# Performance work log

Hardware: AMD Instinct MI355X
Metric: run time of the kernel (lower is better)

Reference implementation:

```python
import jax, jax.numpy as jnp
import numpy as np


def setup_inputs() -> dict:
    key = jax.random.key(0)
    k1, k2 = jax.random.split(key)
    B, T, D = 32, 8192, 256
    enc_hid_states = jax.random.normal(k1, (B, T, D), dtype=jnp.float32)
    dec_hid = jax.random.normal(k2, (B, D), dtype=jnp.float32)
    return {"enc_hid_states": enc_hid_states, "dec_hid": dec_hid}


def reference(enc_hid_states, dec_hid):
    # scores[b, t] = dec_hid[b] . enc_hid_states[b, t]
    scores = jnp.einsum("btd,bd->bt", enc_hid_states, dec_hid)
    align = jax.nn.softmax(scores, axis=1)            # [B, T]
    c_t = jnp.einsum("bt,btd->bd", align, enc_hid_states)  # [B, D]
    return c_t
```

## Files before the change

kernel.cpp:

```cpp
#include <hip/hip_runtime.h>
#include <math.h>


#define WAVES_PER_BLOCK 4
#define BLOCK 256
#define D 256

__global__ __launch_bounds__(BLOCK) void attn_partial(
    const float* __restrict__ enc,
    const float* __restrict__ dec,
    float* __restrict__ ws,
    int T, int P, int nblk_total)
{
    const int blk   = blockIdx.x;
    const int b     = blk / P;
    const int chunk = blk % P;
    const int tid   = threadIdx.x;
    const int wave  = tid >> 6;
    const int lane  = tid & 63;

    const int rows_per_block = T / P;
    const int rows_per_wave  = rows_per_block / WAVES_PER_BLOCK;
    const int t0 = chunk * rows_per_block + wave * rows_per_wave;

    const float* __restrict__ encb = enc + (size_t)b * T * D;

    const float4 dq = *reinterpret_cast<const float4*>(dec + b * D + lane * 4);

    float  m = -INFINITY;
    float  l = 0.0f;
    float4 acc = {0.0f, 0.0f, 0.0f, 0.0f};

    for (int r = 0; r < rows_per_wave; ++r) {
        const int t = t0 + r;
        const float4 x = *reinterpret_cast<const float4*>(encb + (size_t)t * D + lane * 4);
        float p = dq.x * x.x + dq.y * x.y + dq.z * x.z + dq.w * x.w;
        #pragma unroll
        for (int off = 32; off >= 1; off >>= 1)
            p += __shfl_xor(p, off, 64);
        const float mn    = fmaxf(m, p);
        const float scale = __expf(m - mn);
        const float w     = __expf(p - mn);
        acc.x = acc.x * scale + w * x.x;
        acc.y = acc.y * scale + w * x.y;
        acc.z = acc.z * scale + w * x.z;
        acc.w = acc.w * scale + w * x.w;
        l = l * scale + w;
        m = mn;
    }

    __shared__ float s_acc[WAVES_PER_BLOCK][D];
    __shared__ float s_m[WAVES_PER_BLOCK];
    __shared__ float s_l[WAVES_PER_BLOCK];

    *reinterpret_cast<float4*>(&s_acc[wave][lane * 4]) = acc;
    if (lane == 0) { s_m[wave] = m; s_l[wave] = l; }
    __syncthreads();

    if (wave == 0) {
        const float M = fmaxf(fmaxf(s_m[0], s_m[1]), fmaxf(s_m[2], s_m[3]));
        float4 a = {0.0f, 0.0f, 0.0f, 0.0f};
        float  L = 0.0f;
        #pragma unroll
        for (int wv = 0; wv < WAVES_PER_BLOCK; ++wv) {
            const float e = __expf(s_m[wv] - M);
            const float4 aw = *reinterpret_cast<const float4*>(&s_acc[wv][lane * 4]);
            a.x += e * aw.x; a.y += e * aw.y; a.z += e * aw.z; a.w += e * aw.w;
            L += e * s_l[wv];
        }
        float* pacc = ws + (size_t)blk * D;
        *reinterpret_cast<float4*>(pacc + lane * 4) = a;
        if (lane == 0) {
            float* ml = ws + (size_t)nblk_total * D;
            ml[blk * 2 + 0] = M;
            ml[blk * 2 + 1] = L;
        }
    }
}

__global__ __launch_bounds__(BLOCK) void attn_combine(
    const float* __restrict__ ws,
    float* __restrict__ out,
    int P, int nblk_total)
{
    const int b = blockIdx.x;
    const int d = threadIdx.x;
    const float* __restrict__ ml = ws + (size_t)nblk_total * D;

    float M = -INFINITY;
    for (int i = 0; i < P; ++i)
        M = fmaxf(M, ml[(b * P + i) * 2 + 0]);

    float a = 0.0f, L = 0.0f;
    for (int i = 0; i < P; ++i) {
        const int blk = b * P + i;
        const float e = __expf(ml[blk * 2 + 0] - M);
        a += e * ws[(size_t)blk * D + d];
        L += e * ml[blk * 2 + 1];
    }
    out[b * D + d] = a / L;
}

extern "C" void kernel_launch(void* const* d_in, const int* in_sizes, int n_in,
                              void* d_out, int out_size, void* d_ws, size_t ws_size,
                              hipStream_t stream) {
    const float* enc = (const float*)d_in[0];
    const float* dec = (const float*)d_in[1];
    float* out = (float*)d_out;
    float* ws  = (float*)d_ws;

    const int B = in_sizes[1] / D;
    const int T = in_sizes[0] / in_sizes[1];

    int P = 64;
    while (P > 1 && ((size_t)B * P * (D + 2) * sizeof(float)) > ws_size) P >>= 1;
    while (P > 1 && (T % (P * WAVES_PER_BLOCK) != 0)) P >>= 1;

    const int nblk = B * P;
    attn_partial<<<nblk, BLOCK, 0, stream>>>(enc, dec, ws, T, P, nblk);
    attn_combine<<<B, BLOCK, 0, stream>>>(ws, out, P, nblk);
}
```

Measured before the change: 68.42 us.

## Process four rows per wave with 16-lane groups and per-wave partials

Each wave is split into four 16-lane groups that each handle one row per iteration, so a wave loads four rows at once. The 64-lane dot-product shuffle chain shrinks to four shuffles. Rows are interleaved across waves, and each wave writes its own partial after a cross-group shuffle merge, which removes the shared-memory block reduction and the __syncthreads. The combine kernel now splits columns across four blocks per batch and slices the partials across waves. In exchange the partial kernel uses more registers (launch bounds 8), and the combine stage has four times as many partials to read.

Result: slower. 84.75 us (+23.9%).

```diff
diff --git a/kernel.cpp b/kernel.cpp
--- a/kernel.cpp
+++ b/kernel.cpp
@@ -2,15 +2,16 @@
 #include <math.h>
 
 
-#define WAVES_PER_BLOCK 4
 #define BLOCK 256
 #define D 256
+#define WPB 4
+#define ROWS_PER_ITER 16
 
-__global__ __launch_bounds__(BLOCK) void attn_partial(
+__global__ __launch_bounds__(BLOCK, 8) void attn_partial(
     const float* __restrict__ enc,
     const float* __restrict__ dec,
     float* __restrict__ ws,
-    int T, int P, int nblk_total)
+    int T, int P, int nw_total)
 {
     const int blk   = blockIdx.x;
     const int b     = blk / P;
@@ -18,87 +19,132 @@
     const int tid   = threadIdx.x;
     const int wave  = tid >> 6;
     const int lane  = tid & 63;
+    const int g     = lane >> 4;
+    const int k     = lane & 15;
 
     const int rows_per_block = T / P;
-    const int rows_per_wave  = rows_per_block / WAVES_PER_BLOCK;
-    const int t0 = chunk * rows_per_block + wave * rows_per_wave;
+    const int iters = rows_per_block / ROWS_PER_ITER;
+    const int base = chunk * rows_per_block + wave * 4 + g;
 
     const float* __restrict__ encb = enc + (size_t)b * T * D;
+    const float* __restrict__ decb = dec + (size_t)b * D;
 
-    const float4 dq = *reinterpret_cast<const float4*>(dec + b * D + lane * 4);
+    const float4 dq0 = *reinterpret_cast<const float4*>(decb + 0 * 64 + k * 4);
+    const float4 dq1 = *reinterpret_cast<const float4*>(decb + 1 * 64 + k * 4);
+    const float4 dq2 = *reinterpret_cast<const float4*>(decb + 2 * 64 + k * 4);
+    const float4 dq3 = *reinterpret_cast<const float4*>(decb + 3 * 64 + k * 4);
 
     float  m = -INFINITY;
     float  l = 0.0f;
-    float4 acc = {0.0f, 0.0f, 0.0f, 0.0f};
+    float4 a0 = {0,0,0,0}, a1 = {0,0,0,0}, a2 = {0,0,0,0}, a3 = {0,0,0,0};
 
-    for (int r = 0; r < rows_per_wave; ++r) {
-        const int t = t0 + r;
-        const float4 x = *reinterpret_cast<const float4*>(encb + (size_t)t * D + lane * 4);
-        float p = dq.x * x.x + dq.y * x.y + dq.z * x.z + dq.w * x.w;
-        #pragma unroll
-        for (int off = 32; off >= 1; off >>= 1)
-            p += __shfl_xor(p, off, 64);
+    const float* rowp = encb + (size_t)base * D + k * 4;
+
+    for (int i = 0; i < iters; ++i) {
+        const float* rp = rowp + (size_t)i * ROWS_PER_ITER * D;
+        const float4 x0 = *reinterpret_cast<const float4*>(rp + 0 * 64);
+        const float4 x1 = *reinterpret_cast<const float4*>(rp + 1 * 64);
+        const float4 x2 = *reinterpret_cast<const float4*>(rp + 2 * 64);
+        const float4 x3 = *reinterpret_cast<const float4*>(rp + 3 * 64);
+
+        float p = x0.x*dq0.x + x0.y*dq0.y + x0.z*dq0.z + x0.w*dq0.w;
+        p = fmaf(x1.x, dq1.x, fmaf(x1.y, dq1.y, fmaf(x1.z, dq1.z, fmaf(x1.w, dq1.w, p))));
+        p = fmaf(x2.x, dq2.x, fmaf(x2.y, dq2.y, fmaf(x2.z, dq2.z, fmaf(x2.w, dq2.w, p))));
+        p = fmaf(x3.x, dq3.x, fmaf(x3.y, dq3.y, fmaf(x3.z, dq3.z, fmaf(x3.w, dq3.w, p))));
+
+        p += __shfl_xor(p, 1, 64);
+        p += __shfl_xor(p, 2, 64);
+        p += __shfl_xor(p, 4, 64);
+        p += __shfl_xor(p, 8, 64);
+
         const float mn    = fmaxf(m, p);
         const float scale = __expf(m - mn);
         const float w     = __expf(p - mn);
-        acc.x = acc.x * scale + w * x.x;
-        acc.y = acc.y * scale + w * x.y;
-        acc.z = acc.z * scale + w * x.z;
-        acc.w = acc.w * scale + w * x.w;
-        l = l * scale + w;
+
+        a0.x = fmaf(w, x0.x, a0.x * scale); a0.y = fmaf(w, x0.y, a0.y * scale);
+        a0.z = fmaf(w, x0.z, a0.z * scale); a0.w = fmaf(w, x0.w, a0.w * scale);
+        a1.x = fmaf(w, x1.x, a1.x * scale); a1.y = fmaf(w, x1.y, a1.y * scale);
+        a1.z = fmaf(w, x1.z, a1.z * scale); a1.w = fmaf(w, x1.w, a1.w * scale);
+        a2.x = fmaf(w, x2.x, a2.x * scale); a2.y = fmaf(w, x2.y, a2.y * scale);
+        a2.z = fmaf(w, x2.z, a2.z * scale); a2.w = fmaf(w, x2.w, a2.w * scale);
+        a3.x = fmaf(w, x3.x, a3.x * scale); a3.y = fmaf(w, x3.y, a3.y * scale);
+        a3.z = fmaf(w, x3.z, a3.z * scale); a3.w = fmaf(w, x3.w, a3.w * scale);
+        l = fmaf(l, scale, w);
         m = mn;
     }
 
-    __shared__ float s_acc[WAVES_PER_BLOCK][D];
-    __shared__ float s_m[WAVES_PER_BLOCK];
-    __shared__ float s_l[WAVES_PER_BLOCK];
+    float M = fmaxf(m, __shfl_xor(m, 16, 64));
+    M = fmaxf(M, __shfl_xor(M, 32, 64));
+    const float e = __expf(m - M);
+    l *= e;
+    a0.x *= e; a0.y *= e; a0.z *= e; a0.w *= e;
+    a1.x *= e; a1.y *= e; a1.z *= e; a1.w *= e;
+    a2.x *= e; a2.y *= e; a2.z *= e; a2.w *= e;
+    a3.x *= e; a3.y *= e; a3.z *= e; a3.w *= e;
 
-    *reinterpret_cast<float4*>(&s_acc[wave][lane * 4]) = acc;
-    if (lane == 0) { s_m[wave] = m; s_l[wave] = l; }
-    __syncthreads();
+    l += __shfl_xor(l, 16, 64); l += __shfl_xor(l, 32, 64);
+#define RED2(c) c += __shfl_xor(c, 16, 64); c += __shfl_xor(c, 32, 64)
+    RED2(a0.x); RED2(a0.y); RED2(a0.z); RED2(a0.w);
+    RED2(a1.x); RED2(a1.y); RED2(a1.z); RED2(a1.w);
+    RED2(a2.x); RED2(a2.y); RED2(a2.z); RED2(a2.w);
+    RED2(a3.x); RED2(a3.y); RED2(a3.z); RED2(a3.w);
+#undef RED2
 
-    if (wave == 0) {
-        const float M = fmaxf(fmaxf(s_m[0], s_m[1]), fmaxf(s_m[2], s_m[3]));
-        float4 a = {0.0f, 0.0f, 0.0f, 0.0f};
-        float  L = 0.0f;
-        #pragma unroll
-        for (int wv = 0; wv < WAVES_PER_BLOCK; ++wv) {
-            const float e = __expf(s_m[wv] - M);
-            const float4 aw = *reinterpret_cast<const float4*>(&s_acc[wv][lane * 4]);
-            a.x += e * aw.x; a.y += e * aw.y; a.z += e * aw.z; a.w += e * aw.w;
-            L += e * s_l[wv];
-        }
-        float* pacc = ws + (size_t)blk * D;
-        *reinterpret_cast<float4*>(pacc + lane * 4) = a;
-        if (lane == 0) {
-            float* ml = ws + (size_t)nblk_total * D;
-            ml[blk * 2 + 0] = M;
-            ml[blk * 2 + 1] = L;
-        }
+    const float4 lo = (g & 1) ? a1 : a0;
+    const float4 hi = (g & 1) ? a3 : a2;
+    const float4 v  = (g & 2) ? hi : lo;
+
+    const int wid = blk * WPB + wave;
+    *reinterpret_cast<float4*>(ws + (size_t)wid * D + lane * 4) = v;
+    if (lane == 0) {
+        float* ml = ws + (size_t)nw_total * D;
+        ml[wid * 2 + 0] = M;
+        ml[wid * 2 + 1] = l;
     }
 }
 
 __global__ __launch_bounds__(BLOCK) void attn_combine(
     const float* __restrict__ ws,
     float* __restrict__ out,
-    int P, int nblk_total)
+    int nw, int nw_total)
 {
-    const int b = blockIdx.x;
-    const int d = threadIdx.x;
-    const float* __restrict__ ml = ws + (size_t)nblk_total * D;
+    const int b     = blockIdx.x >> 2;
+    const int cq    = blockIdx.x & 3;
+    const int tid   = threadIdx.x;
+    const int lane  = tid & 63;
+    const int slice = tid >> 6;
+    const int col   = cq * 64 + lane;
+    const int i0    = b * nw;
 
-    float M = -INFINITY;
-    for (int i = 0; i < P; ++i)
-        M = fmaxf(M, ml[(b * P + i) * 2 + 0]);
+    const float* __restrict__ ml = ws + (size_t)nw_total * D;
+
+    __shared__ float sM[4];
+    __shared__ float sL[4];
+    __shared__ float sA[4][64];
+
+    float Mw = -INFINITY;
+    for (int i = slice; i < nw; i += 4)
+        Mw = fmaxf(Mw, ml[(i0 + i) * 2 + 0]);
+    if (lane == 0) sM[slice] = Mw;
+    __syncthreads();
+    const float M = fmaxf(fmaxf(sM[0], sM[1]), fmaxf(sM[2], sM[3]));
 
     float a = 0.0f, L = 0.0f;
-    for (int i = 0; i < P; ++i) {
-        const int blk = b * P + i;
-        const float e = __expf(ml[blk * 2 + 0] - M);
-        a += e * ws[(size_t)blk * D + d];
-        L += e * ml[blk * 2 + 1];
+    for (int i = slice; i < nw; i += 4) {
+        const int pid = i0 + i;
+        const float e = __expf(ml[pid * 2 + 0] - M);
+        a = fmaf(e, ws[(size_t)pid * D + col], a);
+        L = fmaf(e, ml[pid * 2 + 1], L);
     }
-    out[b * D + d] = a / L;
+    sA[slice][lane] = a;
+    if (lane == 0) sL[slice] = L;
+    __syncthreads();
+
+    if (slice == 0) {
+        const float at = sA[0][lane] + sA[1][lane] + sA[2][lane] + sA[3][lane];
+        const float Lt = sL[0] + sL[1] + sL[2] + sL[3];
+        out[b * D + col] = at / Lt;
+    }
 }
 
 extern "C" void kernel_launch(void* const* d_in, const int* in_sizes, int n_in,
@@ -113,10 +159,11 @@
     const int T = in_sizes[0] / in_sizes[1];
 
     int P = 64;
-    while (P > 1 && ((size_t)B * P * (D + 2) * sizeof(float)) > ws_size) P >>= 1;
-    while (P > 1 && (T % (P * WAVES_PER_BLOCK) != 0)) P >>= 1;
+    while (P > 1 && ((size_t)B * P * WPB * (D + 2) * sizeof(float)) > ws_size) P >>= 1;
+    while (P > 1 && (T % (P * ROWS_PER_ITER) != 0)) P >>= 1;
 
-    const int nblk = B * P;
-    attn_partial<<<nblk, BLOCK, 0, stream>>>(enc, dec, ws, T, P, nblk);
-    attn_combine<<<B, BLOCK, 0, stream>>>(ws, out, P, nblk);
+    const int nblk     = B * P;
+    const int nw_total = nblk * WPB;
+    attn_partial<<<nblk, BLOCK, 0, stream>>>(enc, dec, ws, T, P, nw_total);
+    attn_combine<<<B * 4, BLOCK, 0, stream>>>(ws, out, P * WPB, nw_total);
 }
```
